# Performance work log

Hardware: AMD Instinct MI355X
Metric: run time of the kernel (lower is better)

The kernel has to match this reference:

```python
import jax, jax.numpy as jnp
import numpy as np

B = 256      # graphs per batch
N = 512      # nodes per graph
FEAT = 64    # num_features
H = 64       # nhid
DEG = 16     # avg degree
RATIO = 0.5  # pooling_ratio
E = B * N * DEG


def setup_inputs() -> dict:
    key = jax.random.key(0)
    ks = jax.random.split(key, 12)
    # edges constructed within each graph via offsets
    src_loc = jax.random.randint(ks[0], (B, N * DEG), 0, N)
    dst_loc = jax.random.randint(ks[1], (B, N * DEG), 0, N)
    offs = (jnp.arange(B) * N)[:, None]
    edge_src = (src_loc + offs).reshape(-1).astype(jnp.int32)
    edge_dst = (dst_loc + offs).reshape(-1).astype(jnp.int32)
    batch = jnp.repeat(jnp.arange(B, dtype=jnp.int32), N)
    x = jax.random.normal(ks[2], (B * N, FEAT), dtype=jnp.float32)
    edge_attr = jax.random.uniform(ks[3], (E,), dtype=jnp.float32) + 0.1
    s1 = 1.0 / np.sqrt(FEAT)
    s2 = 1.0 / np.sqrt(H)
    return {
        "x": x,
        "edge_attr": edge_attr,
        "W1": jax.random.normal(ks[4], (FEAT, H), jnp.float32) * s1,
        "b1": jnp.zeros((H,), jnp.float32),
        "Wp1": jax.random.normal(ks[5], (H, 1), jnp.float32) * s2,
        "bp1": jnp.zeros((1,), jnp.float32),
        "W2": jax.random.normal(ks[6], (H, H), jnp.float32) * s2,
        "b2": jnp.zeros((H,), jnp.float32),
        "Wp2": jax.random.normal(ks[7], (H, 1), jnp.float32) * s2,
        "bp2": jnp.zeros((1,), jnp.float32),
        "edge_src": edge_src,
        "edge_dst": edge_dst,
        "batch": batch,
    }


def gcn_conv(x, W, b, src, dst, ew, n):
    """PyG GCNConv: sym-normalized weighted adjacency + self-loops (weight 1)."""
    h = x @ W                                   # [n, out]
    deg = jnp.zeros((n,), x.dtype).at[dst].add(ew) + 1.0  # self-loop adds 1
    dinv = jax.lax.rsqrt(deg)
    coef = dinv[dst] * ew * dinv[src]           # [E]
    out = jnp.zeros_like(h).at[dst].add(coef[:, None] * h[src])
    out = out + h * (1.0 / deg)[:, None]        # self-loop term: deg^-0.5 * 1 * deg^-0.5
    return out + b


def sag_pool(x, src, dst, ew, Wp, bp, n_per):
    """SAGPool: score = GCNConv(x)->1, per-graph top-k, gate by tanh(score),
    filter edges (dropped edges represented by zero weight)."""
    n = x.shape[0]
    score = gcn_conv(x, Wp, bp, src, dst, ew, n)[:, 0]   # [n]
    k = int(np.ceil(RATIO * n_per))
    _, idx = jax.lax.top_k(score.reshape(B, n_per), k)   # [B, k] local indices
    perm = (idx + (jnp.arange(B) * n_per)[:, None]).reshape(-1)
    xn = x[perm] * jnp.tanh(score[perm])[:, None]        # [B*k, H]
    newid = jnp.full((n,), -1, jnp.int32).at[perm].set(
        jnp.arange(B * k, dtype=jnp.int32))
    ns, nd = newid[src], newid[dst]
    valid = (ns >= 0) & (nd >= 0)
    ew2 = jnp.where(valid, ew, 0.0)
    ns = jnp.where(valid, ns, 0)
    nd = jnp.where(valid, nd, 0)
    return xn, ns, nd, ew2, k


def readout(x, k):
    """[gmp || gap] per graph; each graph has exactly k nodes, contiguous."""
    xg = x.reshape(B, k, -1)
    return jnp.concatenate([xg.max(axis=1), xg.mean(axis=1)], axis=1)  # [B, 2H]


def reference(x, edge_attr, W1, b1, Wp1, bp1, W2, b2, Wp2, bp2,
              edge_src, edge_dst, batch):
    n0 = x.shape[0]
    h = jax.nn.relu(gcn_conv(x, W1, b1, edge_src, edge_dst, edge_attr, n0))
    h, s1, d1, w1e, k1 = sag_pool(h, edge_src, edge_dst, edge_attr, Wp1, bp1, N)
    x1 = readout(h, k1)
    h = jax.nn.relu(gcn_conv(h, W2, b2, s1, d1, w1e, B * k1))
    h, _, _, _, k2 = sag_pool(h, s1, d1, w1e, Wp2, bp2, k1)
    x2 = readout(h, k2)
    return (x1 + x2) / 2.0
```

## Files before the change

kernel.cpp:

```cpp
#include <hip/hip_runtime.h>
#include <math.h>

#define BG   256
#define NN   512
#define EPG  (NN * 16)
#define NE   (BG * EPG)

__device__ __forceinline__ float4 f4fma(float s, float4 a, float4 c) {
    c.x = fmaf(s, a.x, c.x); c.y = fmaf(s, a.y, c.y);
    c.z = fmaf(s, a.z, c.z); c.w = fmaf(s, a.w, c.w);
    return c;
}

__device__ __forceinline__ void gemm_tile(const float* __restrict__ shx,
                                          const float4* __restrict__ W4,
                                          int row0, int rg, int cg, float4 a[4]) {
    float4 acc0 = make_float4(0.f, 0.f, 0.f, 0.f);
    float4 acc1 = acc0, acc2 = acc0, acc3 = acc0;
#pragma unroll
    for (int k4 = 0; k4 < 16; ++k4) {
        float4 xv0 = *(const float4*)&shx[(row0 + rg * 4 + 0) * 68 + k4 * 4];
        float4 xv1 = *(const float4*)&shx[(row0 + rg * 4 + 1) * 68 + k4 * 4];
        float4 xv2 = *(const float4*)&shx[(row0 + rg * 4 + 2) * 68 + k4 * 4];
        float4 xv3 = *(const float4*)&shx[(row0 + rg * 4 + 3) * 68 + k4 * 4];
        float4 wv0 = W4[(k4 * 4 + 0) * 16 + cg];
        float4 wv1 = W4[(k4 * 4 + 1) * 16 + cg];
        float4 wv2 = W4[(k4 * 4 + 2) * 16 + cg];
        float4 wv3 = W4[(k4 * 4 + 3) * 16 + cg];
        acc0 = f4fma(xv0.x, wv0, acc0); acc0 = f4fma(xv0.y, wv1, acc0);
        acc0 = f4fma(xv0.z, wv2, acc0); acc0 = f4fma(xv0.w, wv3, acc0);
        acc1 = f4fma(xv1.x, wv0, acc1); acc1 = f4fma(xv1.y, wv1, acc1);
        acc1 = f4fma(xv1.z, wv2, acc1); acc1 = f4fma(xv1.w, wv3, acc1);
        acc2 = f4fma(xv2.x, wv0, acc2); acc2 = f4fma(xv2.y, wv1, acc2);
        acc2 = f4fma(xv2.z, wv2, acc2); acc2 = f4fma(xv2.w, wv3, acc2);
        acc3 = f4fma(xv3.x, wv0, acc3); acc3 = f4fma(xv3.y, wv1, acc3);
        acc3 = f4fma(xv3.z, wv2, acc3); acc3 = f4fma(xv3.w, wv3, acc3);
    }
    a[0] = acc0; a[1] = acc1; a[2] = acc2; a[3] = acc3;
}

__global__ __launch_bounds__(1024)
void mega_kernel(const int* __restrict__ esrc, const int* __restrict__ edst,
                 const float* __restrict__ eatt, int2* __restrict__ pairs,
                 const float4* __restrict__ X4,
                 const float4* __restrict__ W1_4, const float4* __restrict__ b1_4,
                 const float4* __restrict__ wp1_4, const float* __restrict__ bp1,
                 const float4* __restrict__ W2_4, const float4* __restrict__ b2_4,
                 const float4* __restrict__ wp2_4, const float* __restrict__ bp2,
                 float* __restrict__ out) {
    __shared__ __align__(16) float smem[40720];
    float* shx  = smem;
    float* S    = smem + 34816;
    int*   cnt   = (int*)S;
    int*   rstl  = (int*)S + 512;
    float* sdinv = S + 1024;
    int*   perm  = (int*)S + 1536;
    int*   scn   = (int*)S + 2048;
    float* shp   = S + 2048;
    float* wsum  = S + 2560;
    float* ssc   = S + 2560;
    int*   rnk   = (int*)S + 3072;
    float* sbw   = S + 3584;
    int*   hist  = (int*)S + 3648;
    int*   wtot  = (int*)S + 3712;
    float* x1rs  = S + 3728;
    float4* redx = (float4*)(S + 3856);

    int g = blockIdx.x, nb1 = g * NN, e0 = g * EPG;
    int t = threadIdx.x;
    int lane16 = t & 15, lane = t & 63;

    for (int i = t; i < NN; i += 1024) { cnt[i] = 0; wsum[i] = 0.f; }
    __syncthreads();
    {
        const int4*   edst4 = (const int4*)(edst + e0);
        const int4*   esrc4 = (const int4*)(esrc + e0);
        const float4* eatt4 = (const float4*)(eatt + e0);
        int ed[8], es[8]; float ea[8];
#pragma unroll
        for (int c = 0; c < 2; ++c) {
            int ch = t + c * 1024;
            int4 dd = edst4[ch]; int4 ss = esrc4[ch]; float4 ww = eatt4[ch];
            ed[c*4+0]=dd.x; ed[c*4+1]=dd.y; ed[c*4+2]=dd.z; ed[c*4+3]=dd.w;
            es[c*4+0]=ss.x; es[c*4+1]=ss.y; es[c*4+2]=ss.z; es[c*4+3]=ss.w;
            ea[c*4+0]=ww.x; ea[c*4+1]=ww.y; ea[c*4+2]=ww.z; ea[c*4+3]=ww.w;
        }
#pragma unroll
        for (int j = 0; j < 8; ++j) {
            int dl = ed[j] - nb1;
            atomicAdd(&cnt[dl], 1);
            atomicAdd(&wsum[dl], ea[j]);
        }
        __syncthreads();
        int wv = t >> 6;
        int xval = (t < NN) ? cnt[t] : 0;
        int xs = xval;
#pragma unroll
        for (int off = 1; off < 64; off <<= 1) {
            int v = __shfl_up(xs, off, 64);
            if (lane >= off) xs += v;
        }
        if (lane == 63) wtot[wv] = xs;
        __syncthreads();
        int woff = 0;
#pragma unroll
        for (int w = 0; w < 16; ++w) { int wt = wtot[w]; if (w < wv) woff += wt; }
        xs += woff;
        if (t < NN) {
            int st = xs - xval;
            rstl[t] = st;
            sdinv[t] = rsqrtf(wsum[t] + 1.0f);
            scn[t] = st;
        }
        __syncthreads();
        int slots[8]; float cf[8];
#pragma unroll
        for (int j = 0; j < 8; ++j) {
            int dl = ed[j] - nb1, sl = es[j] - nb1;
            cf[j] = sdinv[dl] * ea[j] * sdinv[sl];
            slots[j] = atomicAdd(&scn[dl], 1);
        }
        int2* lp = (int2*)smem;
#pragma unroll
        for (int j = 0; j < 8; ++j)
            if (slots[j] < 4096)
                lp[slots[j]] = make_int2(es[j] - nb1, __float_as_int(cf[j]));
        __syncthreads();
        for (int k = t; k < 4096; k += 1024) pairs[e0 + k] = lp[k];
        __syncthreads();
#pragma unroll
        for (int j = 0; j < 8; ++j)
            if (slots[j] >= 4096)
                lp[slots[j] - 4096] = make_int2(es[j] - nb1, __float_as_int(cf[j]));
        __syncthreads();
        for (int k = t; k < 4096; k += 1024) pairs[e0 + 4096 + k] = lp[k];
        __syncthreads();
    }
    for (int i = t; i < NN * 16; i += 1024) {
        int r = i >> 4, c4 = i & 15;
        *(float4*)&shx[r * 68 + c4 * 4] = X4[(size_t)nb1 * 16 + i];
    }
    if (t < 64) { sbw[t] = ((const float*)b1_4)[t]; hist[t] = 0; }
    for (int i = t; i < NN; i += 1024) rnk[i] = 0;
    __syncthreads();
    {
        int q = t >> 8, tq = t & 255, rg = tq >> 4, cg = tq & 15;
        float4 ac[2][4];
#pragma unroll
        for (int tt = 0; tt < 2; ++tt)
            gemm_tile(shx, W1_4, (tt * 4 + q) * 64, rg, cg, ac[tt]);
        __syncthreads();
#pragma unroll
        for (int tt = 0; tt < 2; ++tt) {
            int row0 = (tt * 4 + q) * 64;
            *(float4*)&shx[(row0 + rg * 4 + 0) * 68 + cg * 4] = ac[tt][0];
            *(float4*)&shx[(row0 + rg * 4 + 1) * 68 + cg * 4] = ac[tt][1];
            *(float4*)&shx[(row0 + rg * 4 + 2) * 68 + cg * 4] = ac[tt][2];
            *(float4*)&shx[(row0 + rg * 4 + 3) * 68 + cg * 4] = ac[tt][3];
        }
    }
    __syncthreads();
    for (int i = t; i < NN; i += 1024) atomicAdd(&hist[min(cnt[i], 63)], 1);
    __syncthreads();
    if (t < 64) {
        int v = hist[t], s = v;
#pragma unroll
        for (int off = 1; off < 64; off <<= 1) {
            int u = __shfl_up(s, off, 64);
            if (lane >= off) s += u;
        }
        hist[t] = s - v;
    }
    __syncthreads();
    for (int i = t; i < NN; i += 1024) {
        int pos = atomicAdd(&hist[min(cnt[i], 63)], 1);
        perm[pos] = i;
    }
    __syncthreads();
    {
        int idx2 = t >> 1, half = t & 1, fb = half * 8;
        int nl = perm[idx2];
        int st = rstl[nl], cn = cnt[nl];
        float di = sdinv[nl], dii = di * di;
        const int2* pb = pairs + e0 + st;
        float4 acc[8];
#pragma unroll
        for (int c = 0; c < 8; ++c) {
            float4 xv = *(const float4*)&shx[nl * 68 + (fb + c) * 4];
            acc[c].x = fmaf(xv.x, dii, sbw[(fb + c) * 4 + 0]);
            acc[c].y = fmaf(xv.y, dii, sbw[(fb + c) * 4 + 1]);
            acc[c].z = fmaf(xv.z, dii, sbw[(fb + c) * 4 + 2]);
            acc[c].w = fmaf(xv.w, dii, sbw[(fb + c) * 4 + 3]);
        }
        int2 p0 = (cn > 0) ? pb[0] : make_int2(0, 0);
        int2 p1 = (cn > 1) ? pb[1] : make_int2(0, 0);
        for (int j = 0; j < cn; ++j) {
            int2 p2 = (j + 2 < cn) ? pb[j + 2] : make_int2(0, 0);
            float cfv = __int_as_float(p0.y);
            int   s   = p0.x;
#pragma unroll
            for (int c = 0; c < 8; ++c)
                acc[c] = f4fma(cfv, *(const float4*)&shx[s * 68 + (fb + c) * 4], acc[c]);
            p0 = p1; p1 = p2;
        }
#pragma unroll
        for (int c = 0; c < 8; ++c) {
            acc[c].x = fmaxf(acc[c].x, 0.f); acc[c].y = fmaxf(acc[c].y, 0.f);
            acc[c].z = fmaxf(acc[c].z, 0.f); acc[c].w = fmaxf(acc[c].w, 0.f);
        }
        __syncthreads();
#pragma unroll
        for (int c = 0; c < 8; ++c)
            *(float4*)&shx[nl * 68 + (fb + c) * 4] = acc[c];
    }
    __syncthreads();
    if (t < 512) {
        int wv8 = t >> 6, sub4 = (t >> 4) & 3;
        float4 w4 = wp1_4[lane16];
#pragma unroll
        for (int p = 0; p < 16; ++p) {
            int n2 = p * 32 + wv8 * 4 + sub4;
            float4 a = *(const float4*)&shx[n2 * 68 + lane16 * 4];
            float tt = a.x * w4.x + a.y * w4.y + a.z * w4.z + a.w * w4.w;
            tt += __shfl_xor(tt, 1, 64); tt += __shfl_xor(tt, 2, 64);
            tt += __shfl_xor(tt, 4, 64); tt += __shfl_xor(tt, 8, 64);
            if (lane16 == 0) shp[n2] = tt;
        }
    }
    __syncthreads();
    if (t < NN) {
        int i = perm[t];
        int st = rstl[i], cn = cnt[i];
        float di = sdinv[i];
        const int2* pb = pairs + e0 + st;
        float a = fmaf(shp[i], di * di, bp1[0]);
        int2 q0 = (cn > 0) ? pb[0] : make_int2(0, 0);
        int2 q1 = (cn > 1) ? pb[1] : make_int2(0, 0);
        for (int j = 0; j < cn; ++j) {
            int2 q2v = (j + 2 < cn) ? pb[j + 2] : make_int2(0, 0);
            a = fmaf(__int_as_float(q0.y), shp[q0.x], a);
            q0 = q1; q1 = q2v;
        }
        ssc[i] = a;
    }
    __syncthreads();
    {
        int part = t >> 9, i = t & 511;
        float si = ssc[i];
        int j0 = part * 256, rank = 0;
        for (int j = j0; j < j0 + 256; j += 4) {
            float4 sj = *(const float4*)&ssc[j];
            rank += (sj.x > si) || (sj.x == si && j     < i);
            rank += (sj.y > si) || (sj.y == si && j + 1 < i);
            rank += (sj.z > si) || (sj.z == si && j + 2 < i);
            rank += (sj.w > si) || (sj.w == si && j + 3 < i);
        }
        atomicAdd(&rnk[i], rank);
    }
    __syncthreads();
    {
        float4 mx = make_float4(-3.402823466e38f, -3.402823466e38f, -3.402823466e38f, -3.402823466e38f);
        float4 sm = make_float4(0.f, 0.f, 0.f, 0.f);
        if (t < 512) {
            int wv8 = t >> 6, sub4 = (t >> 4) & 3;
#pragma unroll
            for (int p = 0; p < 16; ++p) {
                int n2 = p * 32 + wv8 * 4 + sub4;
                int r = rnk[n2];
                if (r < 256) {
                    float gt = tanhf(ssc[n2]);
                    float4 v = *(const float4*)&shx[n2 * 68 + lane16 * 4];
                    v.x *= gt; v.y *= gt; v.z *= gt; v.w *= gt;
                    mx.x = fmaxf(mx.x, v.x); mx.y = fmaxf(mx.y, v.y);
                    mx.z = fmaxf(mx.z, v.z); mx.w = fmaxf(mx.w, v.w);
                    sm.x += v.x; sm.y += v.y; sm.z += v.z; sm.w += v.w;
                }
            }
        }
        int grp = t >> 4;
        __syncthreads();
        if (t < 512) redx[grp * 16 + lane16] = mx;
        __syncthreads();
        float mr[4] = {0, 0, 0, 0};
        if (grp == 0) {
#pragma unroll
            for (int u = 1; u < 32; ++u) {
                float4 a = redx[u * 16 + lane16];
                mx.x = fmaxf(mx.x, a.x); mx.y = fmaxf(mx.y, a.y);
                mx.z = fmaxf(mx.z, a.z); mx.w = fmaxf(mx.w, a.w);
            }
            mr[0] = mx.x; mr[1] = mx.y; mr[2] = mx.z; mr[3] = mx.w;
        }
        __syncthreads();
        if (t < 512) redx[grp * 16 + lane16] = sm;
        __syncthreads();
        if (grp == 0) {
#pragma unroll
            for (int u = 1; u < 32; ++u) {
                float4 b = redx[u * 16 + lane16];
                sm.x += b.x; sm.y += b.y; sm.z += b.z; sm.w += b.w;
            }
            float invK = 1.f / 256.f;
            int c = lane16 * 4;
            float ar[4] = {sm.x * invK, sm.y * invK, sm.z * invK, sm.w * invK};
#pragma unroll
            for (int u = 0; u < 4; ++u) {
                x1rs[c + u]      = mr[u];
                x1rs[64 + c + u] = ar[u];
            }
        }
    }
    {
        int* nor = perm;
        __syncthreads();
        for (int i = t; i < NN; i += 1024) {
            int r = rnk[i];
            if (r < 256) nor[r] = i;
        }
        __syncthreads();
        float4 stash[4];
        int rr[4], cc[4];
#pragma unroll
        for (int u = 0; u < 4; ++u) {
            int idx = t + u * 1024;
            rr[u] = idx >> 4; cc[u] = idx & 15;
            int n = nor[rr[u]];
            float gt = tanhf(ssc[n]);
            float4 v = *(const float4*)&shx[n * 68 + cc[u] * 4];
            v.x *= gt; v.y *= gt; v.z *= gt; v.w *= gt;
            stash[u] = v;
        }
        __syncthreads();
#pragma unroll
        for (int u = 0; u < 4; ++u)
            *(float4*)&shx[rr[u] * 68 + cc[u] * 4] = stash[u];
        __syncthreads();
    }

    int2* lp2 = (int2*)&shx[256 * 68];
    for (int i = t; i < 256; i += 1024) { cnt[i] = 0; wsum[i] = 0.f; }
    __syncthreads();
    {
        const int4*   edst4 = (const int4*)(edst + e0);
        const int4*   esrc4 = (const int4*)(esrc + e0);
        const float4* eatt4 = (const float4*)(eatt + e0);
        int ed[8], es[8]; float ea[8];
#pragma unroll
        for (int c = 0; c < 2; ++c) {
            int ch = t + c * 1024;
            int4 dd = edst4[ch]; int4 ss = esrc4[ch]; float4 ww = eatt4[ch];
            ed[c*4+0]=dd.x; ed[c*4+1]=dd.y; ed[c*4+2]=dd.z; ed[c*4+3]=dd.w;
            es[c*4+0]=ss.x; es[c*4+1]=ss.y; es[c*4+2]=ss.z; es[c*4+3]=ss.w;
            ea[c*4+0]=ww.x; ea[c*4+1]=ww.y; ea[c*4+2]=ww.z; ea[c*4+3]=ww.w;
        }
#pragma unroll
        for (int j = 0; j < 8; ++j) {
            int rd = rnk[ed[j] - nb1], rs = rnk[es[j] - nb1];
            ed[j] = (rd < 256) ? rd : -1;
            es[j] = (rs < 256) ? rs : -1;
        }
#pragma unroll
        for (int j = 0; j < 8; ++j) {
            if (ed[j] >= 0 && es[j] >= 0) {
                atomicAdd(&cnt[ed[j]], 1);
                atomicAdd(&wsum[ed[j]], ea[j]);
            }
        }
        __syncthreads();
        int wv = t >> 6;
        int xval = (t < 256) ? cnt[t] : 0;
        int xs = xval;
#pragma unroll
        for (int off = 1; off < 64; off <<= 1) {
            int v = __shfl_up(xs, off, 64);
            if (lane >= off) xs += v;
        }
        if (lane == 63) wtot[wv] = xs;
        __syncthreads();
        int woff = 0;
#pragma unroll
        for (int w = 0; w < 16; ++w) { int wt = wtot[w]; if (w < wv) woff += wt; }
        xs += woff;
        if (t < 256) {
            int st = xs - xval;
            rstl[t] = st;
            sdinv[t] = rsqrtf(wsum[t] + 1.0f);
            scn[t] = st;
        }
        __syncthreads();
        int slots[8]; float cf[8];
#pragma unroll
        for (int j = 0; j < 8; ++j) {
            slots[j] = -1;
            if (ed[j] >= 0 && es[j] >= 0) {
                cf[j] = sdinv[ed[j]] * ea[j] * sdinv[es[j]];
                slots[j] = atomicAdd(&scn[ed[j]], 1);
            }
        }
#pragma unroll
        for (int j = 0; j < 8; ++j)
            if (slots[j] >= 0)
                lp2[slots[j]] = make_int2(es[j], __float_as_int(cf[j]));
        for (int i = t; i < 256; i += 1024) rnk[i] = 0;
        if (t < 64) { sbw[t] = ((const float*)b2_4)[t]; hist[t] = 0; }
        __syncthreads();
    }
    {
        int q = t >> 8, tq = t & 255, rg = tq >> 4, cg = tq & 15;
        float4 a4[4];
        gemm_tile(shx, W2_4, q * 64, rg, cg, a4);
        __syncthreads();
        int row0 = q * 64;
        *(float4*)&shx[(row0 + rg * 4 + 0) * 68 + cg * 4] = a4[0];
        *(float4*)&shx[(row0 + rg * 4 + 1) * 68 + cg * 4] = a4[1];
        *(float4*)&shx[(row0 + rg * 4 + 2) * 68 + cg * 4] = a4[2];
        *(float4*)&shx[(row0 + rg * 4 + 3) * 68 + cg * 4] = a4[3];
    }
    __syncthreads();
    for (int i = t; i < 256; i += 1024) atomicAdd(&hist[min(cnt[i], 63)], 1);
    __syncthreads();
    if (t < 64) {
        int v = hist[t], s = v;
#pragma unroll
        for (int off = 1; off < 64; off <<= 1) {
            int u = __shfl_up(s, off, 64);
            if (lane >= off) s += u;
        }
        hist[t] = s - v;
    }
    __syncthreads();
    for (int i = t; i < 256; i += 1024) {
        int pos = atomicAdd(&hist[min(cnt[i], 63)], 1);
        perm[pos] = i;
    }
    __syncthreads();
    {
        int idx2 = t >> 2, half = t & 3, fb = half * 4;
        int nl = perm[idx2];
        int st = rstl[nl], cn = cnt[nl];
        float di = sdinv[nl], dii = di * di;
        const int2* pb = lp2 + st;
        float4 acc[4];
#pragma unroll
        for (int c = 0; c < 4; ++c) {
            float4 xv = *(const float4*)&shx[nl * 68 + (fb + c) * 4];
            acc[c].x = fmaf(xv.x, dii, sbw[(fb + c) * 4 + 0]);
            acc[c].y = fmaf(xv.y, dii, sbw[(fb + c) * 4 + 1]);
            acc[c].z = fmaf(xv.z, dii, sbw[(fb + c) * 4 + 2]);
            acc[c].w = fmaf(xv.w, dii, sbw[(fb + c) * 4 + 3]);
        }
        int2 p0 = (cn > 0) ? pb[0] : make_int2(0, 0);
        int2 p1 = (cn > 1) ? pb[1] : make_int2(0, 0);
        for (int j = 0; j < cn; ++j) {
            int2 p2 = (j + 2 < cn) ? pb[j + 2] : make_int2(0, 0);
            float cfv = __int_as_float(p0.y);
            int   s   = p0.x;
#pragma unroll
            for (int c = 0; c < 4; ++c)
                acc[c] = f4fma(cfv, *(const float4*)&shx[s * 68 + (fb + c) * 4], acc[c]);
            p0 = p1; p1 = p2;
        }
#pragma unroll
        for (int c = 0; c < 4; ++c) {
            acc[c].x = fmaxf(acc[c].x, 0.f); acc[c].y = fmaxf(acc[c].y, 0.f);
            acc[c].z = fmaxf(acc[c].z, 0.f); acc[c].w = fmaxf(acc[c].w, 0.f);
        }
        __syncthreads();
#pragma unroll
        for (int c = 0; c < 4; ++c)
            *(float4*)&shx[nl * 68 + (fb + c) * 4] = acc[c];
    }
    __syncthreads();
    if (t < 512) {
        int wv8 = t >> 6, sub4 = (t >> 4) & 3;
        float4 w4 = wp2_4[lane16];
#pragma unroll
        for (int p = 0; p < 8; ++p) {
            int n2 = p * 32 + wv8 * 4 + sub4;
            float4 a = *(const float4*)&shx[n2 * 68 + lane16 * 4];
            float tt = a.x * w4.x + a.y * w4.y + a.z * w4.z + a.w * w4.w;
            tt += __shfl_xor(tt, 1, 64); tt += __shfl_xor(tt, 2, 64);
            tt += __shfl_xor(tt, 4, 64); tt += __shfl_xor(tt, 8, 64);
            if (lane16 == 0) shp[n2] = tt;
        }
    }
    __syncthreads();
    if (t < 256) {
        int i = perm[t];
        int st = rstl[i], cn = cnt[i];
        float di = sdinv[i];
        const int2* pb = lp2 + st;
        float a = fmaf(shp[i], di * di, bp2[0]);
        int2 q0 = (cn > 0) ? pb[0] : make_int2(0, 0);
        int2 q1 = (cn > 1) ? pb[1] : make_int2(0, 0);
        for (int j = 0; j < cn; ++j) {
            int2 q2v = (j + 2 < cn) ? pb[j + 2] : make_int2(0, 0);
            a = fmaf(__int_as_float(q0.y), shp[q0.x], a);
            q0 = q1; q1 = q2v;
        }
        ssc[i] = a;
    }
    __syncthreads();
    {
        int part = t >> 8, i = t & 255;
        float si = ssc[i];
        int j0 = part * 64, rank = 0;
        for (int j = j0; j < j0 + 64; j += 4) {
            float4 sj = *(const float4*)&ssc[j];
            rank += (sj.x > si) || (sj.x == si && j     < i);
            rank += (sj.y > si) || (sj.y == si && j + 1 < i);
            rank += (sj.z > si) || (sj.z == si && j + 2 < i);
            rank += (sj.w > si) || (sj.w == si && j + 3 < i);
        }
        atomicAdd(&rnk[i], rank);
    }
    __syncthreads();
    {
        float4 mx = make_float4(-3.402823466e38f, -3.402823466e38f, -3.402823466e38f, -3.402823466e38f);
        float4 sm = make_float4(0.f, 0.f, 0.f, 0.f);
        if (t < 512) {
            int wv8 = t >> 6, sub4 = (t >> 4) & 3;
#pragma unroll
            for (int p = 0; p < 8; ++p) {
                int n2 = p * 32 + wv8 * 4 + sub4;
                int r = rnk[n2];
                if (r < 128) {
                    float gt = tanhf(ssc[n2]);
                    float4 v = *(const float4*)&shx[n2 * 68 + lane16 * 4];
                    v.x *= gt; v.y *= gt; v.z *= gt; v.w *= gt;
                    mx.x = fmaxf(mx.x, v.x); mx.y = fmaxf(mx.y, v.y);
                    mx.z = fmaxf(mx.z, v.z); mx.w = fmaxf(mx.w, v.w);
                    sm.x += v.x; sm.y += v.y; sm.z += v.z; sm.w += v.w;
                }
            }
        }
        int grp = t >> 4;
        __syncthreads();
        if (t < 512) redx[grp * 16 + lane16] = mx;
        __syncthreads();
        float mr[4] = {0, 0, 0, 0};
        if (grp == 0) {
#pragma unroll
            for (int u = 1; u < 32; ++u) {
                float4 a = redx[u * 16 + lane16];
                mx.x = fmaxf(mx.x, a.x); mx.y = fmaxf(mx.y, a.y);
                mx.z = fmaxf(mx.z, a.z); mx.w = fmaxf(mx.w, a.w);
            }
            mr[0] = mx.x; mr[1] = mx.y; mr[2] = mx.z; mr[3] = mx.w;
        }
        __syncthreads();
        if (t < 512) redx[grp * 16 + lane16] = sm;
        __syncthreads();
        if (grp == 0) {
#pragma unroll
            for (int u = 1; u < 32; ++u) {
                float4 b = redx[u * 16 + lane16];
                sm.x += b.x; sm.y += b.y; sm.z += b.z; sm.w += b.w;
            }
            float invK = 1.f / 128.f;
            int c = lane16 * 4;
            float ar[4] = {sm.x * invK, sm.y * invK, sm.z * invK, sm.w * invK};
#pragma unroll
            for (int u = 0; u < 4; ++u) {
                out[g * 128 + c + u]      = 0.5f * (x1rs[c + u]      + mr[u]);
                out[g * 128 + 64 + c + u] = 0.5f * (x1rs[64 + c + u] + ar[u]);
            }
        }
    }
}

extern "C" void kernel_launch(void* const* d_in, const int* in_sizes, int n_in,
                              void* d_out, int out_size, void* d_ws, size_t ws_size,
                              hipStream_t stream) {
    const float* x    = (const float*)d_in[0];
    const float* eatt = (const float*)d_in[1];
    const float* W1   = (const float*)d_in[2];
    const float* b1   = (const float*)d_in[3];
    const float* Wp1  = (const float*)d_in[4];
    const float* bp1  = (const float*)d_in[5];
    const float* W2   = (const float*)d_in[6];
    const float* b2   = (const float*)d_in[7];
    const float* Wp2  = (const float*)d_in[8];
    const float* bp2  = (const float*)d_in[9];
    const int*   esrc = (const int*)d_in[10];
    const int*   edst = (const int*)d_in[11];
    float* out = (float*)d_out;

    int2* prs = (int2*)d_ws;

    mega_kernel<<<BG, 1024, 0, stream>>>(
        esrc, edst, eatt, prs, (const float4*)x,
        (const float4*)W1, (const float4*)b1, (const float4*)Wp1, bp1,
        (const float4*)W2, (const float4*)b2, (const float4*)Wp2, bp2,
        out);
}
```

Before: 209.9 us.

## Warp-specialize block: overlap CSR build with X load and GEMM tiles

Splits the 1024-thread block into two halves. The first 512 threads build the CSR adjacency (degree counts, scan, slot scatter), while the other 512 load X into shared memory and run the feature GEMM tiles in the same phases. The second layer's CSR build is overlapped the same way with the gating and the W2 GEMM. The edge list is now staged in one pass into a shared buffer placed after row 256, so the two-pass split through smem is gone. Each half does twice the per-thread work, which raises register pressure and may lengthen the critical path if the two sides are unbalanced.

After: 371.3 us. 76.9% more time.

```diff
diff --git a/kernel.cpp b/kernel.cpp
--- a/kernel.cpp
+++ b/kernel.cpp
@@ -65,116 +65,144 @@
     int*   wtot  = (int*)S + 3712;
     float* x1rs  = S + 3728;
     float4* redx = (float4*)(S + 3856);
+    float* wsum2 = S + 3856;
+    int2*  lp    = (int2*)&shx[256 * 68];
 
     int g = blockIdx.x, nb1 = g * NN, e0 = g * EPG;
     int t = threadIdx.x;
     int lane16 = t & 15, lane = t & 63;
-
-    for (int i = t; i < NN; i += 1024) { cnt[i] = 0; wsum[i] = 0.f; }
-    __syncthreads();
-    {
+    bool csrw = t < 512;
+    int tl = t - 512;
+    int q2 = (t & 511) >> 8, tqq = t & 255, rgg = tqq >> 4, cgg = tqq & 15;
+
+    int ed[16], es[16]; float ea[16];
+    int xs = 0, xval = 0, wv = t >> 6;
+    float4 xreg[8];
+    float4 ac[2][4];
+
+    if (csrw) {
+        cnt[t] = 0; wsum[t] = 0.f;
+    } else {
+#pragma unroll
+        for (int u = 0; u < 8; ++u) {
+            int idx = tl + u * 512;
+            *(float4*)&shx[(idx >> 4) * 68 + (idx & 15) * 4] = X4[(size_t)nb1 * 16 + idx];
+        }
+        if (tl < 64) { sbw[tl] = ((const float*)b1_4)[tl]; hist[tl] = 0; }
+        rnk[tl] = 0;
+    }
+    __syncthreads();
+    if (csrw) {
         const int4*   edst4 = (const int4*)(edst + e0);
         const int4*   esrc4 = (const int4*)(esrc + e0);
         const float4* eatt4 = (const float4*)(eatt + e0);
-        int ed[8], es[8]; float ea[8];
-#pragma unroll
-        for (int c = 0; c < 2; ++c) {
-            int ch = t + c * 1024;
+#pragma unroll
+        for (int c = 0; c < 4; ++c) {
+            int ch = t + c * 512;
             int4 dd = edst4[ch]; int4 ss = esrc4[ch]; float4 ww = eatt4[ch];
             ed[c*4+0]=dd.x; ed[c*4+1]=dd.y; ed[c*4+2]=dd.z; ed[c*4+3]=dd.w;
             es[c*4+0]=ss.x; es[c*4+1]=ss.y; es[c*4+2]=ss.z; es[c*4+3]=ss.w;
             ea[c*4+0]=ww.x; ea[c*4+1]=ww.y; ea[c*4+2]=ww.z; ea[c*4+3]=ww.w;
         }
 #pragma unroll
-        for (int j = 0; j < 8; ++j) {
+        for (int j = 0; j < 16; ++j) {
             int dl = ed[j] - nb1;
             atomicAdd(&cnt[dl], 1);
             atomicAdd(&wsum[dl], ea[j]);
         }
-        __syncthreads();
-        int wv = t >> 6;
-        int xval = (t < NN) ? cnt[t] : 0;
-        int xs = xval;
+    } else {
+#pragma unroll
+        for (int tt = 0; tt < 2; ++tt)
+            gemm_tile(shx, W1_4, (tt * 2 + q2) * 64, rgg, cgg, ac[tt]);
+    }
+    __syncthreads();
+    if (csrw) {
+        xval = cnt[t];
+        xs = xval;
 #pragma unroll
         for (int off = 1; off < 64; off <<= 1) {
             int v = __shfl_up(xs, off, 64);
             if (lane >= off) xs += v;
         }
         if (lane == 63) wtot[wv] = xs;
-        __syncthreads();
+    } else {
+#pragma unroll
+        for (int tt = 0; tt < 2; ++tt) {
+            int row0 = (tt * 2 + q2) * 64;
+            *(float4*)&shx[(row0 + rgg * 4 + 0) * 68 + cgg * 4] = ac[tt][0];
+            *(float4*)&shx[(row0 + rgg * 4 + 1) * 68 + cgg * 4] = ac[tt][1];
+            *(float4*)&shx[(row0 + rgg * 4 + 2) * 68 + cgg * 4] = ac[tt][2];
+            *(float4*)&shx[(row0 + rgg * 4 + 3) * 68 + cgg * 4] = ac[tt][3];
+        }
+    }
+    __syncthreads();
+    if (csrw) {
         int woff = 0;
 #pragma unroll
-        for (int w = 0; w < 16; ++w) { int wt = wtot[w]; if (w < wv) woff += wt; }
+        for (int w = 0; w < 8; ++w) { int wt = wtot[w]; if (w < wv) woff += wt; }
         xs += woff;
-        if (t < NN) {
-            int st = xs - xval;
-            rstl[t] = st;
-            sdinv[t] = rsqrtf(wsum[t] + 1.0f);
-            scn[t] = st;
-        }
-        __syncthreads();
-        int slots[8]; float cf[8];
-#pragma unroll
-        for (int j = 0; j < 8; ++j) {
+        int st = xs - xval;
+        rstl[t] = st;
+        sdinv[t] = rsqrtf(wsum[t] + 1.0f);
+        scn[t] = st;
+    } else {
+#pragma unroll
+        for (int u = 0; u < 8; ++u)
+            xreg[u] = X4[(size_t)nb1 * 16 + 4096 + tl + u * 512];
+    }
+    __syncthreads();
+    if (csrw) {
+#pragma unroll
+        for (int j = 0; j < 16; ++j) {
             int dl = ed[j] - nb1, sl = es[j] - nb1;
-            cf[j] = sdinv[dl] * ea[j] * sdinv[sl];
-            slots[j] = atomicAdd(&scn[dl], 1);
-        }
-        int2* lp = (int2*)smem;
-#pragma unroll
-        for (int j = 0; j < 8; ++j)
-            if (slots[j] < 4096)
-                lp[slots[j]] = make_int2(es[j] - nb1, __float_as_int(cf[j]));
-        __syncthreads();
-        for (int k = t; k < 4096; k += 1024) pairs[e0 + k] = lp[k];
-        __syncthreads();
-#pragma unroll
-        for (int j = 0; j < 8; ++j)
-            if (slots[j] >= 4096)
-                lp[slots[j] - 4096] = make_int2(es[j] - nb1, __float_as_int(cf[j]));
-        __syncthreads();
-        for (int k = t; k < 4096; k += 1024) pairs[e0 + 4096 + k] = lp[k];
-        __syncthreads();
-    }
-    for (int i = t; i < NN * 16; i += 1024) {
-        int r = i >> 4, c4 = i & 15;
-        *(float4*)&shx[r * 68 + c4 * 4] = X4[(size_t)nb1 * 16 + i];
-    }
-    if (t < 64) { sbw[t] = ((const float*)b1_4)[t]; hist[t] = 0; }
-    for (int i = t; i < NN; i += 1024) rnk[i] = 0;
-    __syncthreads();
-    {
-        int q = t >> 8, tq = t & 255, rg = tq >> 4, cg = tq & 15;
-        float4 ac[2][4];
-#pragma unroll
-        for (int tt = 0; tt < 2; ++tt)
-            gemm_tile(shx, W1_4, (tt * 4 + q) * 64, rg, cg, ac[tt]);
-        __syncthreads();
+            float cf = sdinv[dl] * ea[j] * sdinv[sl];
+            int slot = atomicAdd(&scn[dl], 1);
+            lp[slot] = make_int2(sl, __float_as_int(cf));
+        }
+    }
+    __syncthreads();
+    for (int k = t; k < EPG; k += 1024) pairs[e0 + k] = lp[k];
+    __syncthreads();
+    if (!csrw) {
+#pragma unroll
+        for (int u = 0; u < 8; ++u) {
+            int idx = 4096 + tl + u * 512;
+            *(float4*)&shx[(idx >> 4) * 68 + (idx & 15) * 4] = xreg[u];
+        }
+    }
+    __syncthreads();
+    if (csrw) {
+        atomicAdd(&hist[min(cnt[t], 63)], 1);
+    } else {
+        gemm_tile(shx, W1_4, (4 + q2) * 64, rgg, cgg, ac[0]);
+    }
+    __syncthreads();
+    if (csrw) {
+        if (t < 64) {
+            int v = hist[t], s = v;
+#pragma unroll
+            for (int off = 1; off < 64; off <<= 1) {
+                int u = __shfl_up(s, off, 64);
+                if (lane >= off) s += u;
+            }
+            hist[t] = s - v;
+        }
+    } else {
+        gemm_tile(shx, W1_4, (6 + q2) * 64, rgg, cgg, ac[1]);
+    }
+    __syncthreads();
+    if (csrw) {
+        int pos = atomicAdd(&hist[min(cnt[t], 63)], 1);
+        perm[pos] = t;
+    } else {
 #pragma unroll
         for (int tt = 0; tt < 2; ++tt) {
-            int row0 = (tt * 4 + q) * 64;
-            *(float4*)&shx[(row0 + rg * 4 + 0) * 68 + cg * 4] = ac[tt][0];
-            *(float4*)&shx[(row0 + rg * 4 + 1) * 68 + cg * 4] = ac[tt][1];
-            *(float4*)&shx[(row0 + rg * 4 + 2) * 68 + cg * 4] = ac[tt][2];
-            *(float4*)&shx[(row0 + rg * 4 + 3) * 68 + cg * 4] = ac[tt][3];
-        }
-    }
-    __syncthreads();
-    for (int i = t; i < NN; i += 1024) atomicAdd(&hist[min(cnt[i], 63)], 1);
-    __syncthreads();
-    if (t < 64) {
-        int v = hist[t], s = v;
-#pragma unroll
-        for (int off = 1; off < 64; off <<= 1) {
-            int u = __shfl_up(s, off, 64);
-            if (lane >= off) s += u;
-        }
-        hist[t] = s - v;
-    }
-    __syncthreads();
-    for (int i = t; i < NN; i += 1024) {
-        int pos = atomicAdd(&hist[min(cnt[i], 63)], 1);
-        perm[pos] = i;
+            int row0 = (4 + tt * 2 + q2) * 64;
+            *(float4*)&shx[(row0 + rgg * 4 + 0) * 68 + cgg * 4] = ac[tt][0];
+            *(float4*)&shx[(row0 + rgg * 4 + 1) * 68 + cgg * 4] = ac[tt][1];
+            *(float4*)&shx[(row0 + rgg * 4 + 2) * 68 + cgg * 4] = ac[tt][2];
+            *(float4*)&shx[(row0 + rgg * 4 + 3) * 68 + cgg * 4] = ac[tt][3];
+        }
     }
     __syncthreads();
     {
@@ -214,7 +242,7 @@
             *(float4*)&shx[nl * 68 + (fb + c) * 4] = acc[c];
     }
     __syncthreads();
-    if (t < 512) {
+    if (csrw) {
         int wv8 = t >> 6, sub4 = (t >> 4) & 3;
         float4 w4 = wp1_4[lane16];
 #pragma unroll
@@ -261,7 +289,7 @@
     {
         float4 mx = make_float4(-3.402823466e38f, -3.402823466e38f, -3.402823466e38f, -3.402823466e38f);
         float4 sm = make_float4(0.f, 0.f, 0.f, 0.f);
-        if (t < 512) {
+        if (csrw) {
             int wv8 = t >> 6, sub4 = (t >> 4) & 3;
 #pragma unroll
             for (int p = 0; p < 16; ++p) {
@@ -279,7 +307,7 @@
         }
         int grp = t >> 4;
         __syncthreads();
-        if (t < 512) redx[grp * 16 + lane16] = mx;
+        if (csrw) redx[grp * 16 + lane16] = mx;
         __syncthreads();
         float mr[4] = {0, 0, 0, 0};
         if (grp == 0) {
@@ -292,7 +320,7 @@
             mr[0] = mx.x; mr[1] = mx.y; mr[2] = mx.z; mr[3] = mx.w;
         }
         __syncthreads();
-        if (t < 512) redx[grp * 16 + lane16] = sm;
+        if (csrw) redx[grp * 16 + lane16] = sm;
         __syncthreads();
         if (grp == 0) {
 #pragma unroll
@@ -310,128 +338,133 @@
             }
         }
     }
-    {
-        int* nor = perm;
-        __syncthreads();
-        for (int i = t; i < NN; i += 1024) {
-            int r = rnk[i];
-            if (r < 256) nor[r] = i;
-        }
-        __syncthreads();
-        float4 stash[4];
-        int rr[4], cc[4];
-#pragma unroll
-        for (int u = 0; u < 4; ++u) {
-            int idx = t + u * 1024;
-            rr[u] = idx >> 4; cc[u] = idx & 15;
-            int n = nor[rr[u]];
-            float gt = tanhf(ssc[n]);
-            float4 v = *(const float4*)&shx[n * 68 + cc[u] * 4];
-            v.x *= gt; v.y *= gt; v.z *= gt; v.w *= gt;
-            stash[u] = v;
-        }
-        __syncthreads();
-#pragma unroll
-        for (int u = 0; u < 4; ++u)
-            *(float4*)&shx[rr[u] * 68 + cc[u] * 4] = stash[u];
-        __syncthreads();
-    }
-
-    int2* lp2 = (int2*)&shx[256 * 68];
-    for (int i = t; i < 256; i += 1024) { cnt[i] = 0; wsum[i] = 0.f; }
-    __syncthreads();
-    {
+    __syncthreads();
+
+    if (csrw) {
+        if (t < 256) { cnt[t] = 0; wsum2[t] = 0.f; }
         const int4*   edst4 = (const int4*)(edst + e0);
         const int4*   esrc4 = (const int4*)(esrc + e0);
         const float4* eatt4 = (const float4*)(eatt + e0);
-        int ed[8], es[8]; float ea[8];
-#pragma unroll
-        for (int c = 0; c < 2; ++c) {
-            int ch = t + c * 1024;
+#pragma unroll
+        for (int c = 0; c < 4; ++c) {
+            int ch = t + c * 512;
             int4 dd = edst4[ch]; int4 ss = esrc4[ch]; float4 ww = eatt4[ch];
             ed[c*4+0]=dd.x; ed[c*4+1]=dd.y; ed[c*4+2]=dd.z; ed[c*4+3]=dd.w;
             es[c*4+0]=ss.x; es[c*4+1]=ss.y; es[c*4+2]=ss.z; es[c*4+3]=ss.w;
             ea[c*4+0]=ww.x; ea[c*4+1]=ww.y; ea[c*4+2]=ww.z; ea[c*4+3]=ww.w;
         }
 #pragma unroll
-        for (int j = 0; j < 8; ++j) {
+        for (int j = 0; j < 16; ++j) {
             int rd = rnk[ed[j] - nb1], rs = rnk[es[j] - nb1];
             ed[j] = (rd < 256) ? rd : -1;
             es[j] = (rs < 256) ? rs : -1;
         }
-#pragma unroll
-        for (int j = 0; j < 8; ++j) {
+    } else {
+        int r = rnk[tl];
+        if (r < 256) perm[r] = tl;
+    }
+    __syncthreads();
+    if (csrw) {
+#pragma unroll
+        for (int j = 0; j < 16; ++j) {
             if (ed[j] >= 0 && es[j] >= 0) {
                 atomicAdd(&cnt[ed[j]], 1);
-                atomicAdd(&wsum[ed[j]], ea[j]);
-            }
-        }
-        __syncthreads();
-        int wv = t >> 6;
-        int xval = (t < 256) ? cnt[t] : 0;
-        int xs = xval;
-#pragma unroll
-        for (int off = 1; off < 64; off <<= 1) {
-            int v = __shfl_up(xs, off, 64);
-            if (lane >= off) xs += v;
-        }
-        if (lane == 63) wtot[wv] = xs;
-        __syncthreads();
-        int woff = 0;
-#pragma unroll
-        for (int w = 0; w < 16; ++w) { int wt = wtot[w]; if (w < wv) woff += wt; }
-        xs += woff;
+                atomicAdd(&wsum2[ed[j]], ea[j]);
+            }
+        }
+    } else {
+#pragma unroll
+        for (int u = 0; u < 8; ++u) {
+            int idx = tl + u * 512;
+            int n = perm[idx >> 4];
+            float gt = tanhf(ssc[n]);
+            float4 v = *(const float4*)&shx[n * 68 + (idx & 15) * 4];
+            v.x *= gt; v.y *= gt; v.z *= gt; v.w *= gt;
+            xreg[u] = v;
+        }
+    }
+    __syncthreads();
+    if (csrw) {
         if (t < 256) {
+            xval = cnt[t];
+            xs = xval;
+#pragma unroll
+            for (int off = 1; off < 64; off <<= 1) {
+                int v = __shfl_up(xs, off, 64);
+                if (lane >= off) xs += v;
+            }
+            if (lane == 63) wtot[wv] = xs;
+        }
+    } else {
+#pragma unroll
+        for (int u = 0; u < 8; ++u) {
+            int idx = tl + u * 512;
+            *(float4*)&shx[(idx >> 4) * 68 + (idx & 15) * 4] = xreg[u];
+        }
+    }
+    __syncthreads();
+    if (csrw) {
+        if (t < 256) {
+            int woff = 0;
+#pragma unroll
+            for (int w = 0; w < 4; ++w) { int wt = wtot[w]; if (w < wv) woff += wt; }
+            xs += woff;
             int st = xs - xval;
             rstl[t] = st;
-            sdinv[t] = rsqrtf(wsum[t] + 1.0f);
+            sdinv[t] = rsqrtf(wsum2[t] + 1.0f);
             scn[t] = st;
-        }
-        __syncthreads();
-        int slots[8]; float cf[8];
-#pragma unroll
-        for (int j = 0; j < 8; ++j) {
-            slots[j] = -1;
+        } else {
+            rnk[t & 255] = 0;
+        }
+        if (t < 64) { sbw[t] = ((const float*)b2_4)[t]; hist[t] = 0; }
+    } else {
+        gemm_tile(shx, W2_4, q2 * 64, rgg, cgg, ac[0]);
+    }
+    __syncthreads();
+    if (csrw) {
+#pragma unroll
+        for (int j = 0; j < 16; ++j) {
             if (ed[j] >= 0 && es[j] >= 0) {
-                cf[j] = sdinv[ed[j]] * ea[j] * sdinv[es[j]];
-                slots[j] = atomicAdd(&scn[ed[j]], 1);
-            }
-        }
-#pragma unroll
-        for (int j = 0; j < 8; ++j)
-            if (slots[j] >= 0)
-                lp2[slots[j]] = make_int2(es[j], __float_as_int(cf[j]));
-        for (int i = t; i < 256; i += 1024) rnk[i] = 0;
-        if (t < 64) { sbw[t] = ((const float*)b2_4)[t]; hist[t] = 0; }
-        __syncthreads();
-    }
-    {
-        int q = t >> 8, tq = t & 255, rg = tq >> 4, cg = tq & 15;
-        float4 a4[4];
-        gemm_tile(shx, W2_4, q * 64, rg, cg, a4);
-        __syncthreads();
-        int row0 = q * 64;
-        *(float4*)&shx[(row0 + rg * 4 + 0) * 68 + cg * 4] = a4[0];
-        *(float4*)&shx[(row0 + rg * 4 + 1) * 68 + cg * 4] = a4[1];
-        *(float4*)&shx[(row0 + rg * 4 + 2) * 68 + cg * 4] = a4[2];
-        *(float4*)&shx[(row0 + rg * 4 + 3) * 68 + cg * 4] = a4[3];
-    }
-    __syncthreads();
-    for (int i = t; i < 256; i += 1024) atomicAdd(&hist[min(cnt[i], 63)], 1);
-    __syncthreads();
-    if (t < 64) {
-        int v = hist[t], s = v;
-#pragma unroll
-        for (int off = 1; off < 64; off <<= 1) {
-            int u = __shfl_up(s, off, 64);
-            if (lane >= off) s += u;
-        }
-        hist[t] = s - v;
-    }
-    __syncthreads();
-    for (int i = t; i < 256; i += 1024) {
-        int pos = atomicAdd(&hist[min(cnt[i], 63)], 1);
-        perm[pos] = i;
+                float cf = sdinv[ed[j]] * ea[j] * sdinv[es[j]];
+                int slot = atomicAdd(&scn[ed[j]], 1);
+                lp[slot] = make_int2(es[j], __float_as_int(cf));
+            }
+        }
+    } else {
+        int row0 = q2 * 64;
+        *(float4*)&shx[(row0 + rgg * 4 + 0) * 68 + cgg * 4] = ac[0][0];
+        *(float4*)&shx[(row0 + rgg * 4 + 1) * 68 + cgg * 4] = ac[0][1];
+        *(float4*)&shx[(row0 + rgg * 4 + 2) * 68 + cgg * 4] = ac[0][2];
+        *(float4*)&shx[(row0 + rgg * 4 + 3) * 68 + cgg * 4] = ac[0][3];
+    }
+    __syncthreads();
+    if (csrw) {
+        if (t < 256) atomicAdd(&hist[min(cnt[t], 63)], 1);
+    } else {
+        gemm_tile(shx, W2_4, (2 + q2) * 64, rgg, cgg, ac[1]);
+    }
+    __syncthreads();
+    if (csrw) {
+        if (t < 64) {
+            int v = hist[t], s = v;
+#pragma unroll
+            for (int off = 1; off < 64; off <<= 1) {
+                int u = __shfl_up(s, off, 64);
+                if (lane >= off) s += u;
+            }
+            hist[t] = s - v;
+        }
+    } else {
+        int row0 = (2 + q2) * 64;
+        *(float4*)&shx[(row0 + rgg * 4 + 0) * 68 + cgg * 4] = ac[1][0];
+        *(float4*)&shx[(row0 + rgg * 4 + 1) * 68 + cgg * 4] = ac[1][1];
+        *(float4*)&shx[(row0 + rgg * 4 + 2) * 68 + cgg * 4] = ac[1][2];
+        *(float4*)&shx[(row0 + rgg * 4 + 3) * 68 + cgg * 4] = ac[1][3];
+    }
+    __syncthreads();
+    if (t < 256) {
+        int pos = atomicAdd(&hist[min(cnt[t], 63)], 1);
+        perm[pos] = t;
     }
     __syncthreads();
     {
@@ -439,7 +472,7 @@
         int nl = perm[idx2];
         int st = rstl[nl], cn = cnt[nl];
         float di = sdinv[nl], dii = di * di;
-        const int2* pb = lp2 + st;
+        const int2* pb = lp + st;
         float4 acc[4];
 #pragma unroll
         for (int c = 0; c < 4; ++c) {
@@ -471,7 +504,7 @@
             *(float4*)&shx[nl * 68 + (fb + c) * 4] = acc[c];
     }
     __syncthreads();
-    if (t < 512) {
+    if (csrw) {
         int wv8 = t >> 6, sub4 = (t >> 4) & 3;
         float4 w4 = wp2_4[lane16];
 #pragma unroll
@@ -489,7 +522,7 @@
         int i = perm[t];
         int st = rstl[i], cn = cnt[i];
         float di = sdinv[i];
-        const int2* pb = lp2 + st;
+        const int2* pb = lp + st;
         float a = fmaf(shp[i], di * di, bp2[0]);
         int2 q0 = (cn > 0) ? pb[0] : make_int2(0, 0);
         int2 q1 = (cn > 1) ? pb[1] : make_int2(0, 0);
@@ -518,7 +551,7 @@
     {
         float4 mx = make_float4(-3.402823466e38f, -3.402823466e38f, -3.402823466e38f, -3.402823466e38f);
         float4 sm = make_float4(0.f, 0.f, 0.f, 0.f);
-        if (t < 512) {
+        if (csrw) {
             int wv8 = t >> 6, sub4 = (t >> 4) & 3;
 #pragma unroll
             for (int p = 0; p < 8; ++p) {
@@ -536,7 +569,7 @@
         }
         int grp = t >> 4;
         __syncthreads();
-        if (t < 512) redx[grp * 16 + lane16] = mx;
+        if (csrw) redx[grp * 16 + lane16] = mx;
         __syncthreads();
         float mr[4] = {0, 0, 0, 0};
         if (grp == 0) {
@@ -549,7 +582,7 @@
             mr[0] = mx.x; mr[1] = mx.y; mr[2] = mx.z; mr[3] = mx.w;
         }
         __syncthreads();
-        if (t < 512) redx[grp * 16 + lane16] = sm;
+        if (csrw) redx[grp * 16 + lane16] = sm;
         __syncthreads();
         if (grp == 0) {
 #pragma unroll
```
